# Kernel optimization log

Hardware: AMD Instinct MI355X
Metric: run time of the kernel (lower is better)

The kernel has to match this reference:

```python
import jax, jax.numpy as jnp
import numpy as np

GAMMA = 0.6
EPS = 1e-10
T = 20
ALPHA = 2.0
BETA = 1.5
LAM = 2.0
ETA = 10.0
PLACEHOLDER = -1
ENABLE_BONUS = False

B, K, V = 64, 8, 50257


def _nan_to(x, val):
    # torch.nan_to_num(nan=val) replaces only NaN, keeps +-inf
    return jnp.where(jnp.isnan(x), jnp.asarray(val, x.dtype), x)


def _costeer(llm, base, steer):
    # llm/base/steer: [B, V]
    llm_log = jax.nn.log_softmax(_nan_to(llm, -100.0), axis=-1)
    base_log = jax.nn.log_softmax(_nan_to(base, -100.0), axis=-1)
    steer_log = jax.nn.log_softmax(_nan_to(steer, -100.0), axis=-1)
    delta = steer_log - base_log
    delta = jnp.where(jnp.isnan(delta), jnp.zeros((), delta.dtype), delta)

    def body(t, carry):
        q_sum, log_p, prev = carry
        q_sum = q_sum + ALPHA * (log_p - llm_log) + BETA * delta
        t_f = t.astype(llm_log.dtype)
        denom = t_f * LAM + 1.0 / ETA
        lp = (t_f * LAM * llm_log + q_sum + prev / ETA) / denom
        lp = jax.nn.log_softmax(lp, axis=-1)
        return (q_sum, lp, lp)

    q0 = jnp.zeros_like(llm_log)
    _, log_p, _ = jax.lax.fori_loop(1, T + 1, body, (q0, llm_log, llm_log))
    return log_p


def setup_inputs() -> dict:
    key = jax.random.key(0)
    k1, k2, k3, k4, k5, k6 = jax.random.split(key, 6)
    target_logits = jax.random.normal(k1, (B * K, V), dtype=jnp.float32)
    base_logits = jax.random.normal(k2, (B * K, V), dtype=jnp.float32)
    steer_logits = jax.random.normal(k3, (B * K, V), dtype=jnp.float32)
    draft_token_ids = jax.random.randint(k4, (B, K), 0, V, dtype=jnp.int32)
    num_draft_tokens = jax.random.randint(k5, (B,), 1, K + 1, dtype=jnp.int32)
    bonus_token_ids = jax.random.randint(k6, (B,), 0, V, dtype=jnp.int32)
    return {
        "target_logits": target_logits,
        "base_logits": base_logits,
        "steer_logits": steer_logits,
        "draft_token_ids": draft_token_ids,
        "num_draft_tokens": num_draft_tokens,
        "bonus_token_ids": bonus_token_ids,
    }


def reference(target_logits, base_logits, steer_logits, draft_token_ids,
              num_draft_tokens, bonus_token_ids):
    tl = target_logits.reshape(B, K, V)
    bl = base_logits.reshape(B, K, V)
    sl = steer_logits.reshape(B, K, V)

    target_probs = jax.nn.softmax(tl, axis=-1)
    base_probs = jax.nn.softmax(bl, axis=-1)

    idx = draft_token_ids[..., None]  # [B, K, 1]
    p_llm = jnp.take_along_axis(target_probs, idx, axis=-1)[..., 0]  # [B, K]
    p_base = jnp.take_along_axis(base_probs, idx, axis=-1)[..., 0]

    pos = jnp.arange(K, dtype=jnp.int32)[None, :]           # [1, K]
    valid = pos < num_draft_tokens[:, None]                  # [B, K]
    accept = (p_llm > GAMMA * (p_base + EPS)) & valid
    prefix = jnp.cumprod(accept.astype(jnp.int32), axis=1)   # 1 until first reject
    cnt = prefix.sum(axis=1).astype(jnp.int32)               # accepted count [B]
    rejected = cnt < num_draft_tokens                        # [B]

    # gather the (first-rejected) row per request; clamp for fully-accepted reqs
    rp = jnp.minimum(cnt, K - 1)[:, None, None]              # [B,1,1]
    llm_r = jnp.take_along_axis(tl, rp, axis=1)[:, 0]        # [B, V]
    base_r = jnp.take_along_axis(bl, rp, axis=1)[:, 0]
    steer_r = jnp.take_along_axis(sl, rp, axis=1)[:, 0]

    fused = _costeer(llm_r, base_r, steer_r)                 # [B, V]
    recovered = jnp.argmax(fused, axis=-1).astype(jnp.int32)  # [B]

    ph = jnp.full((B, K), PLACEHOLDER, dtype=jnp.int32)
    out_main = jnp.where(pos < cnt[:, None], draft_token_ids,
                         jnp.where((pos == cnt[:, None]) & rejected[:, None],
                                   recovered[:, None], ph))  # [B, K]

    if ENABLE_BONUS:
        bonus_col = jnp.where(~rejected, bonus_token_ids,
                              jnp.full((B,), PLACEHOLDER, jnp.int32))[:, None]
    else:
        bonus_col = jnp.full((B, 1), PLACEHOLDER, dtype=jnp.int32)
    output_token_ids = jnp.concatenate([out_main, bonus_col], axis=1)  # [B, K+1]

    return output_token_ids, cnt, fused
```

## Files before the change

kernel.cpp:

```cpp
#include <hip/hip_runtime.h>
#include <cstdint>
#include <cstddef>

#define VDIM 50257
#define BNUM 64
#define KNUM 8
#define TITER 20

#define SEGA   12564
#define NSEGA  4
#define SEGF   1572
#define NSEGF  32
#define EPTF   7

__device__ __forceinline__ void upd(float& m, float& s, float x) {
    float d = m - x;
    float e = __expf(-fabsf(d));
    float t1 = (d >= 0.0f) ? 1.0f : e;
    float t2 = (d >= 0.0f) ? e : 1.0f;
    s = fmaf(s, t1, t2);
    m = fmaxf(m, x);
}

__device__ __forceinline__ void comb(float& m, float& s, float mo, float so) {
    float mn = fmaxf(m, mo);
    s = s * __expf(m - mn) + so * __expf(mo - mn);
    m = mn;
}

__device__ __forceinline__ void blockReduceMS(float& m, float& s, float* shm, int tid) {
    int lane = tid & 63, wid = tid >> 6;
    #pragma unroll
    for (int off = 32; off > 0; off >>= 1) {
        float mo = __shfl_down(m, off);
        float so = __shfl_down(s, off);
        comb(m, s, mo, so);
    }
    if (lane == 0) { shm[2 * wid] = m; shm[2 * wid + 1] = s; }
    __syncthreads();
    if (tid == 0) {
        float M = shm[0], S = shm[1];
        #pragma unroll
        for (int w = 1; w < 4; w++) comb(M, S, shm[2 * w], shm[2 * w + 1]);
        shm[0] = M; shm[1] = S;
    }
    __syncthreads();
    m = shm[0]; s = shm[1];
    __syncthreads();
}

__device__ __forceinline__ void blockReduceArgmax(float& v, int& idx, float* shmf, int* shmi, int tid) {
    int lane = tid & 63, wid = tid >> 6;
    #pragma unroll
    for (int off = 32; off > 0; off >>= 1) {
        float vo = __shfl_down(v, off);
        int   io = __shfl_down(idx, off);
        if (vo > v || (vo == v && io < idx)) { v = vo; idx = io; }
    }
    if (lane == 0) { shmf[wid] = v; shmi[wid] = idx; }
    __syncthreads();
    if (tid == 0) {
        #pragma unroll
        for (int w = 1; w < 4; w++)
            if (shmf[w] > v || (shmf[w] == v && shmi[w] < idx)) { v = shmf[w]; idx = shmi[w]; }
        shmf[0] = v; shmi[0] = idx;
    }
    __syncthreads();
    v = shmf[0]; idx = shmi[0];
    __syncthreads();
}

__global__ __launch_bounds__(256) void k_stats(
        const float* __restrict__ tgt, const float* __restrict__ bse,
        const int* __restrict__ ndraft,
        float* __restrict__ pm_a, float* __restrict__ ps_a) {
    int bid  = blockIdx.x;
    int task = bid >> 2, seg = bid & 3;
    int which = task >> 9, r = task & 511;
    if ((r & 7) >= ndraft[r >> 3]) return;

    const float* row = (which ? bse : tgt) + (size_t)r * VDIM;
    int start = seg * SEGA;
    int len = VDIM - start; if (len > SEGA) len = SEGA;
    const float* p = row + start;
    int tid = threadIdx.x;

    float m0 = -3.0e38f, m1 = -3.0e38f, m2 = -3.0e38f, m3 = -3.0e38f;
    float s0 = 0.f, s1 = 0.f, s2 = 0.f, s3 = 0.f;

    int mis  = (int)(((uintptr_t)p & 15) >> 2);
    int head = (4 - mis) & 3;
    if (tid < head) upd(m0, s0, p[tid]);
    const float4* v4 = (const float4*)(p + head);
    int n4 = (len - head) >> 2;
    for (int g = tid; g < n4; g += 256) {
        float4 x = v4[g];
        upd(m0, s0, x.x); upd(m1, s1, x.y); upd(m2, s2, x.z); upd(m3, s3, x.w);
    }
    int j = head + (n4 << 2) + tid;
    if (j < len) upd(m0, s0, p[j]);

    comb(m0, s0, m1, s1);
    comb(m2, s2, m3, s3);
    comb(m0, s0, m2, s2);

    __shared__ float shm[16];
    blockReduceMS(m0, s0, shm, tid);
    if (tid == 0) { pm_a[bid] = m0; ps_a[bid] = s0; }
}

__global__ __launch_bounds__(1024) void k_accept(
        const float* __restrict__ tgt, const float* __restrict__ bse,
        const int* __restrict__ draft, const int* __restrict__ ndraft,
        const float* __restrict__ pm_a, const float* __restrict__ ps_a,
        float* __restrict__ out_tok, float* __restrict__ out_cnt,
        int* __restrict__ rci ) {
    __shared__ float shp[1024];
    int t = threadIdx.x;
    int which = t >> 9, r = t & 511;
    int b = r >> 3, k = r & 7;

    float pval = 0.0f;
    if (k < ndraft[b]) {
        float M = -3.0e38f, S = 0.0f;
        #pragma unroll
        for (int sg = 0; sg < NSEGA; sg++) comb(M, S, pm_a[t * 4 + sg], ps_a[t * 4 + sg]);
        float lse = M + __logf(S);
        const float* row = (which ? bse : tgt) + (size_t)r * VDIM;
        pval = __expf(row[draft[r]] - lse);
    }
    shp[t] = pval;
    __syncthreads();

    if (t < BNUM) {
        int nd = ndraft[t];
        int cnt = 0; bool chain = true;
        #pragma unroll
        for (int kk = 0; kk < KNUM; kk++) {
            float pl = shp[t * KNUM + kk];
            float pb = shp[512 + t * KNUM + kk];
            bool acc = (kk < nd) && (pl > 0.6f * (pb + 1e-10f));
            chain = chain && acc;
            if (chain) cnt++;
        }
        int rej = (cnt < nd) ? 1 : 0;
        int rp  = cnt < (KNUM - 1) ? cnt : (KNUM - 1);
        #pragma unroll
        for (int kk = 0; kk < KNUM; kk++)
            out_tok[t * (KNUM + 1) + kk] = (kk < cnt) ? (float)draft[t * KNUM + kk] : -1.0f;
        out_tok[t * (KNUM + 1) + KNUM] = -1.0f;
        out_cnt[t] = (float)cnt;
        rci[t] = rp; rci[64 + t] = cnt; rci[128 + t] = rej;
    }
}

__global__ __launch_bounds__(256) void k_fpart(
        const float* __restrict__ tgt, const float* __restrict__ bse,
        const float* __restrict__ str, const int* __restrict__ rci,
        float aa, float bb,
        float* __restrict__ pmf, float* __restrict__ psf,
        float* __restrict__ pvf, int* __restrict__ pif) {
    int blk = blockIdx.x;
    int b = blk >> 5, seg = blk & (NSEGF - 1);
    int tid = threadIdx.x;
    int rp = rci[b];
    size_t roff = (size_t)(b * KNUM + rp) * VDIM;
    const float* tl = tgt + roff;
    const float* bl = bse + roff;
    const float* sl = str + roff;

    int start = seg * SEGF;
    int len = VDIM - start; if (len > SEGF) len = SEGF;

    float m = -3.0e38f, s = 0.0f, bv = -3.0e38f;
    int bi = 0x7fffffff;
    #pragma unroll
    for (int i = 0; i < EPTF; i++) {
        int j = tid + i * 256;
        if (j < len) {
            int g = start + j;
            float y = fmaf(aa, tl[g], bb * (sl[g] - bl[g]));
            upd(m, s, y);
            if (y > bv) { bv = y; bi = g; }
        }
    }
    __shared__ float shm[16];
    __shared__ int   shmi[8];
    blockReduceMS(m, s, shm, tid);
    blockReduceArgmax(bv, bi, shm, shmi, tid);
    if (tid == 0) { pmf[blk] = m; psf[blk] = s; pvf[blk] = bv; pif[blk] = bi; }
}

__global__ __launch_bounds__(256) void k_final(
        const float* __restrict__ tgt, const float* __restrict__ bse,
        const float* __restrict__ str, const int* __restrict__ rci,
        const float* __restrict__ pmf, const float* __restrict__ psf,
        const float* __restrict__ pvf, const int* __restrict__ pif,
        float aa, float bb,
        float* __restrict__ out_tok, float* __restrict__ out_fused) {
    int blk = blockIdx.x;
    int b = blk >> 5, seg = blk & (NSEGF - 1);
    int tid = threadIdx.x;

    __shared__ float shZ;
    __shared__ int   shG;

    if (tid < 64) {
        float M = -3.0e38f, S = 0.0f, V = -3.0e38f;
        int I = 0x7fffffff;
        if (tid < NSEGF) {
            int idx = b * NSEGF + tid;
            M = pmf[idx]; S = psf[idx]; V = pvf[idx]; I = pif[idx];
        }
        #pragma unroll
        for (int off = 32; off > 0; off >>= 1) {
            float Mo = __shfl_down(M, off);
            float So = __shfl_down(S, off);
            float Vo = __shfl_down(V, off);
            int   Io = __shfl_down(I, off);
            comb(M, S, Mo, So);
            if (Vo > V || (Vo == V && Io < I)) { V = Vo; I = Io; }
        }
        if (tid == 0) { shZ = M + __logf(S); shG = I; }
    }
    __syncthreads();
    float Z = shZ;

    int rp = rci[b];
    size_t roff = (size_t)(b * KNUM + rp) * VDIM;
    const float* tl = tgt + roff;
    const float* bl = bse + roff;
    const float* sl = str + roff;

    int start = seg * SEGF;
    int len = VDIM - start; if (len > SEGF) len = SEGF;
    float* dst = out_fused + (size_t)b * VDIM + start;
    #pragma unroll
    for (int i = 0; i < EPTF; i++) {
        int j = tid + i * 256;
        if (j < len) {
            int g = start + j;
            float y = fmaf(aa, tl[g], bb * (sl[g] - bl[g]));
            dst[j] = y - Z;
        }
    }
    if (seg == 0 && tid == 0 && rci[128 + b]) {
        out_tok[b * (KNUM + 1) + rci[64 + b]] = (float)shG;
    }
}


extern "C" void kernel_launch(void* const* d_in, const int* in_sizes, int n_in,
                              void* d_out, int out_size, void* d_ws, size_t ws_size,
                              hipStream_t stream) {
    const float* tgt   = (const float*)d_in[0];
    const float* bse   = (const float*)d_in[1];
    const float* str   = (const float*)d_in[2];
    const int*   draft = (const int*)d_in[3];
    const int*   nd    = (const int*)d_in[4];

    float* out       = (float*)d_out;
    float* out_tok   = out;
    float* out_cnt   = out + BNUM * (KNUM + 1);
    float* out_fused = out + BNUM * (KNUM + 1) + BNUM;

    float* wsf  = (float*)d_ws;
    float* pm_a = wsf;
    float* ps_a = wsf + 4096;
    float* pmf  = wsf + 8192;
    float* psf  = wsf + 10240;
    float* pvf  = wsf + 12288;
    int*   wsi  = (int*)(wsf + 14336);
    int*   rci  = wsi;
    int*   pif  = wsi + 192;

    float dd = 0.0f, ee = 0.0f, aa = 1.0f, bb = 0.0f;
    for (int t = 1; t <= TITER; t++) {
        dd += 2.0f * (aa - 1.0f);
        ee += 2.0f * bb + 1.5f;
        float tf = (float)t;
        float denom = tf * 2.0f + 0.1f;
        float an = (tf * 2.0f + dd + aa * 0.1f) / denom;
        float bn = (ee + bb * 0.1f) / denom;
        aa = an; bb = bn;
    }

    hipLaunchKernelGGL(k_stats, dim3(1024 * NSEGA), dim3(256), 0, stream,
                       tgt, bse, nd, pm_a, ps_a);
    hipLaunchKernelGGL(k_accept, dim3(1), dim3(1024), 0, stream,
                       tgt, bse, draft, nd, pm_a, ps_a, out_tok, out_cnt, rci);
    hipLaunchKernelGGL(k_fpart, dim3(BNUM * NSEGF), dim3(256), 0, stream,
                       tgt, bse, str, rci, aa, bb, pmf, psf, pvf, pif);
    hipLaunchKernelGGL(k_final, dim3(BNUM * NSEGF), dim3(256), 0, stream,
                       tgt, bse, str, rci, pmf, psf, pvf, pif, aa, bb,
                       out_tok, out_fused);
}
```

Measured before the change: 273.8 us.

## Fuse acceptance into partial fused-logit pass and store unnormalized logits

Each partial block now recomputes the acceptance count for its batch row, which removes the single-block acceptance kernel and its launch. The partial pass writes the unnormalized fused logits directly, and a lighter final kernel only subtracts the log-normalizer in place with vectorized float4 accesses. This avoids rereading the three input rows in the final pass. In exchange, 32 blocks per row redundantly recompute the acceptance, and the output is read back and rewritten.

After: 269.0 us. Within noise of the previous version (-1.8%).

```diff
diff --git a/kernel.cpp b/kernel.cpp
--- a/kernel.cpp
+++ b/kernel.cpp
@@ -12,6 +12,8 @@
 #define SEGF   1572
 #define NSEGF  32
 #define EPTF   7
+#define SEGS   6284
+#define NSEGS  8
 
 __device__ __forceinline__ void upd(float& m, float& s, float x) {
     float d = m - x;
@@ -109,61 +111,66 @@
     if (tid == 0) { pm_a[bid] = m0; ps_a[bid] = s0; }
 }
 
-__global__ __launch_bounds__(1024) void k_accept(
+__global__ __launch_bounds__(256) void k_fused(
         const float* __restrict__ tgt, const float* __restrict__ bse,
+        const float* __restrict__ str,
         const int* __restrict__ draft, const int* __restrict__ ndraft,
         const float* __restrict__ pm_a, const float* __restrict__ ps_a,
+        float aa, float bb,
         float* __restrict__ out_tok, float* __restrict__ out_cnt,
-        int* __restrict__ rci ) {
-    __shared__ float shp[1024];
-    int t = threadIdx.x;
-    int which = t >> 9, r = t & 511;
-    int b = r >> 3, k = r & 7;
-
-    float pval = 0.0f;
-    if (k < ndraft[b]) {
-        float M = -3.0e38f, S = 0.0f;
-        #pragma unroll
-        for (int sg = 0; sg < NSEGA; sg++) comb(M, S, pm_a[t * 4 + sg], ps_a[t * 4 + sg]);
-        float lse = M + __logf(S);
-        const float* row = (which ? bse : tgt) + (size_t)r * VDIM;
-        pval = __expf(row[draft[r]] - lse);
-    }
-    shp[t] = pval;
-    __syncthreads();
-
-    if (t < BNUM) {
-        int nd = ndraft[t];
-        int cnt = 0; bool chain = true;
-        #pragma unroll
-        for (int kk = 0; kk < KNUM; kk++) {
-            float pl = shp[t * KNUM + kk];
-            float pb = shp[512 + t * KNUM + kk];
-            bool acc = (kk < nd) && (pl > 0.6f * (pb + 1e-10f));
-            chain = chain && acc;
-            if (chain) cnt++;
-        }
-        int rej = (cnt < nd) ? 1 : 0;
-        int rp  = cnt < (KNUM - 1) ? cnt : (KNUM - 1);
-        #pragma unroll
-        for (int kk = 0; kk < KNUM; kk++)
-            out_tok[t * (KNUM + 1) + kk] = (kk < cnt) ? (float)draft[t * KNUM + kk] : -1.0f;
-        out_tok[t * (KNUM + 1) + KNUM] = -1.0f;
-        out_cnt[t] = (float)cnt;
-        rci[t] = rp; rci[64 + t] = cnt; rci[128 + t] = rej;
-    }
-}
-
-__global__ __launch_bounds__(256) void k_fpart(
-        const float* __restrict__ tgt, const float* __restrict__ bse,
-        const float* __restrict__ str, const int* __restrict__ rci,
-        float aa, float bb,
+        float* __restrict__ out_fused, int* __restrict__ rci,
         float* __restrict__ pmf, float* __restrict__ psf,
         float* __restrict__ pvf, int* __restrict__ pif) {
     int blk = blockIdx.x;
     int b = blk >> 5, seg = blk & (NSEGF - 1);
     int tid = threadIdx.x;
-    int rp = rci[b];
+
+    __shared__ float shp[16];
+    __shared__ float shm[16];
+    __shared__ int   shmi[8];
+    __shared__ int   sh_rp;
+
+    int nd = ndraft[b];
+
+    if (tid < 16) {
+        int which = tid >> 3, k = tid & 7, r = b * KNUM + k;
+        float pval = 0.0f;
+        if (k < nd) {
+            float M = -3.0e38f, S = 0.0f;
+            int base = (which * 512 + r) * NSEGA;
+            #pragma unroll
+            for (int sg = 0; sg < NSEGA; sg++) comb(M, S, pm_a[base + sg], ps_a[base + sg]);
+            float lse = M + __logf(S);
+            const float* row = (which ? bse : tgt) + (size_t)r * VDIM;
+            pval = __expf(row[draft[r]] - lse);
+        }
+        shp[tid] = pval;
+    }
+    __syncthreads();
+    if (tid == 0) {
+        int cnt = 0; bool chain = true;
+        #pragma unroll
+        for (int kk = 0; kk < KNUM; kk++) {
+            float pl = shp[kk], pb = shp[8 + kk];
+            bool acc = (kk < nd) && (pl > 0.6f * (pb + 1e-10f));
+            chain = chain && acc;
+            if (chain) cnt++;
+        }
+        int rej = (cnt < nd) ? 1 : 0;
+        int rp  = cnt < (KNUM - 1) ? cnt : (KNUM - 1);
+        sh_rp = rp;
+        if (seg == 0) {
+            #pragma unroll
+            for (int kk = 0; kk < KNUM; kk++)
+                out_tok[b * (KNUM + 1) + kk] = (kk < cnt) ? (float)draft[b * KNUM + kk] : -1.0f;
+            out_tok[b * (KNUM + 1) + KNUM] = -1.0f;
+            out_cnt[b] = (float)cnt;
+            rci[b] = rp; rci[64 + b] = cnt; rci[128 + b] = rej;
+        }
+    }
+    __syncthreads();
+    int rp = sh_rp;
+
     size_t roff = (size_t)(b * KNUM + rp) * VDIM;
     const float* tl = tgt + roff;
     const float* bl = bse + roff;
@@ -171,6 +178,7 @@
 
     int start = seg * SEGF;
     int len = VDIM - start; if (len > SEGF) len = SEGF;
+    float* dst = out_fused + (size_t)b * VDIM + start;
 
     float m = -3.0e38f, s = 0.0f, bv = -3.0e38f;
     int bi = 0x7fffffff;
@@ -180,26 +188,23 @@
         if (j < len) {
             int g = start + j;
             float y = fmaf(aa, tl[g], bb * (sl[g] - bl[g]));
+            dst[j] = y;
             upd(m, s, y);
             if (y > bv) { bv = y; bi = g; }
         }
     }
-    __shared__ float shm[16];
-    __shared__ int   shmi[8];
     blockReduceMS(m, s, shm, tid);
     blockReduceArgmax(bv, bi, shm, shmi, tid);
     if (tid == 0) { pmf[blk] = m; psf[blk] = s; pvf[blk] = bv; pif[blk] = bi; }
 }
 
-__global__ __launch_bounds__(256) void k_final(
-        const float* __restrict__ tgt, const float* __restrict__ bse,
-        const float* __restrict__ str, const int* __restrict__ rci,
+__global__ __launch_bounds__(256) void k_sub(
+        const int* __restrict__ rci,
         const float* __restrict__ pmf, const float* __restrict__ psf,
         const float* __restrict__ pvf, const int* __restrict__ pif,
-        float aa, float bb,
         float* __restrict__ out_tok, float* __restrict__ out_fused) {
     int blk = blockIdx.x;
-    int b = blk >> 5, seg = blk & (NSEGF - 1);
+    int b = blk >> 3, seg = blk & (NSEGS - 1);
     int tid = threadIdx.x;
 
     __shared__ float shZ;
@@ -213,7 +218,7 @@
             M = pmf[idx]; S = psf[idx]; V = pvf[idx]; I = pif[idx];
         }
         #pragma unroll
-        for (int off = 32; off > 0; off >>= 1) {
+        for (int off = 16; off > 0; off >>= 1) {
             float Mo = __shfl_down(M, off);
             float So = __shfl_down(S, off);
             float Vo = __shfl_down(V, off);
@@ -226,24 +231,24 @@
     __syncthreads();
     float Z = shZ;
 
-    int rp = rci[b];
-    size_t roff = (size_t)(b * KNUM + rp) * VDIM;
-    const float* tl = tgt + roff;
-    const float* bl = bse + roff;
-    const float* sl = str + roff;
-
-    int start = seg * SEGF;
-    int len = VDIM - start; if (len > SEGF) len = SEGF;
-    float* dst = out_fused + (size_t)b * VDIM + start;
-    #pragma unroll
-    for (int i = 0; i < EPTF; i++) {
-        int j = tid + i * 256;
-        if (j < len) {
-            int g = start + j;
-            float y = fmaf(aa, tl[g], bb * (sl[g] - bl[g]));
-            dst[j] = y - Z;
-        }
-    }
+    int start = seg * SEGS;
+    int len = VDIM - start; if (len > SEGS) len = SEGS;
+    float* p = out_fused + (size_t)b * VDIM + start;
+
+    int mis  = (int)(((uintptr_t)p & 15) >> 2);
+    int head = (4 - mis) & 3;
+    if (head > len) head = len;
+    if (tid < head) p[tid] -= Z;
+    float4* v4 = (float4*)(p + head);
+    int n4 = (len - head) >> 2;
+    for (int g = tid; g < n4; g += 256) {
+        float4 x = v4[g];
+        x.x -= Z; x.y -= Z; x.z -= Z; x.w -= Z;
+        v4[g] = x;
+    }
+    int j = head + (n4 << 2) + tid;
+    if (j < len) p[j] -= Z;
+
     if (seg == 0 && tid == 0 && rci[128 + b]) {
         out_tok[b * (KNUM + 1) + rci[64 + b]] = (float)shG;
     }
@@ -287,11 +292,9 @@
 
     hipLaunchKernelGGL(k_stats, dim3(1024 * NSEGA), dim3(256), 0, stream,
                        tgt, bse, nd, pm_a, ps_a);
-    hipLaunchKernelGGL(k_accept, dim3(1), dim3(1024), 0, stream,
-                       tgt, bse, draft, nd, pm_a, ps_a, out_tok, out_cnt, rci);
-    hipLaunchKernelGGL(k_fpart, dim3(BNUM * NSEGF), dim3(256), 0, stream,
-                       tgt, bse, str, rci, aa, bb, pmf, psf, pvf, pif);
-    hipLaunchKernelGGL(k_final, dim3(BNUM * NSEGF), dim3(256), 0, stream,
-                       tgt, bse, str, rci, pmf, psf, pvf, pif, aa, bb,
-                       out_tok, out_fused);
-}
+    hipLaunchKernelGGL(k_fused, dim3(BNUM * NSEGF), dim3(256), 0, stream,
+                       tgt, bse, str, draft, nd, pm_a, ps_a, aa, bb,
+                       out_tok, out_cnt, out_fused, rci, pmf, psf, pvf, pif);
+    hipLaunchKernelGGL(k_sub, dim3(BNUM * NSEGS), dim3(256), 0, stream,
+                       rci, pmf, psf, pvf, pif, out_tok, out_fused);
+}
```
